# Optimization experiments

Measured on AMD Instinct MI355X. Metric: run time of the kernel, lower is better.

## Reference

```python
import jax, jax.numpy as jnp
import numpy as np

N, E = 50000, 1250000
IN_DIM, H, C, EDGE_DIM = 128, 2, 32, 64
NEG_SLOPE = 0.2


def setup_inputs() -> dict:
    key = jax.random.key(0)
    ks = jax.random.split(key, 9)
    x = jax.random.normal(ks[0], (N, IN_DIM), dtype=jnp.float32)
    edge_index = jax.random.randint(ks[1], (2, E), 0, N, dtype=jnp.int64)
    edge_attr = jax.random.normal(ks[2], (E, EDGE_DIM), dtype=jnp.float32)
    # learned params (PyG GATConv: glorot-style scale)
    W = jax.random.normal(ks[3], (IN_DIM, H * C), dtype=jnp.float32) * (1.0 / np.sqrt(IN_DIM))
    W_edge = jax.random.normal(ks[4], (EDGE_DIM, H * C), dtype=jnp.float32) * (1.0 / np.sqrt(EDGE_DIM))
    att_src = jax.random.normal(ks[5], (H, C), dtype=jnp.float32) * (1.0 / np.sqrt(C))
    att_dst = jax.random.normal(ks[6], (H, C), dtype=jnp.float32) * (1.0 / np.sqrt(C))
    att_edge = jax.random.normal(ks[7], (H, C), dtype=jnp.float32) * (1.0 / np.sqrt(C))
    bias = jnp.zeros((H * C,), dtype=jnp.float32)
    return {"x": x, "edge_index": edge_index, "edge_attr": edge_attr,
            "W": W, "W_edge": W_edge, "att_src": att_src, "att_dst": att_dst,
            "att_edge": att_edge, "bias": bias}


def reference(x, edge_index, edge_attr, W, W_edge, att_src, att_dst, att_edge, bias):
    # IntraGraphAttention.forward: relu then GATConv(in, 32, heads=2, edge_dim=64)
    x = jax.nn.relu(x)
    src, dst = edge_index[0], edge_index[1]

    # PyG add_self_loops(fill_value='mean'): self-loop edge_attr = mean of
    # incoming edge attrs per node (zeros for isolated nodes).
    deg = jax.ops.segment_sum(jnp.ones((E,), jnp.float32), dst, num_segments=N)
    loop_attr = jax.ops.segment_sum(edge_attr, dst, num_segments=N) / jnp.maximum(deg, 1.0)[:, None]
    loop_idx = jnp.arange(N, dtype=src.dtype)
    src_f = jnp.concatenate([src, loop_idx])          # [E+N]
    dst_f = jnp.concatenate([dst, loop_idx])          # [E+N]
    eattr_f = jnp.concatenate([edge_attr, loop_attr])  # [E+N, 64]

    # node / edge projections
    h = (x @ W).reshape(N, H, C)                       # [N,H,C]
    a_src = jnp.einsum('nhc,hc->nh', h, att_src)       # [N,H]
    a_dst = jnp.einsum('nhc,hc->nh', h, att_dst)       # [N,H]
    e = (eattr_f @ W_edge).reshape(-1, H, C)           # [E+N,H,C]
    a_edge = jnp.einsum('ehc,hc->eh', e, att_edge)     # [E+N,H]

    # per-edge attention logits
    alpha = a_src[src_f] + a_dst[dst_f] + a_edge       # [E+N,H]
    alpha = jax.nn.leaky_relu(alpha, NEG_SLOPE)

    # segment softmax over destination neighborhoods
    amax = jax.ops.segment_max(alpha, dst_f, num_segments=N)  # [N,H]
    p = jnp.exp(alpha - amax[dst_f])
    denom = jax.ops.segment_sum(p, dst_f, num_segments=N)     # [N,H]
    alpha = p / (denom[dst_f] + 1e-16)

    # scatter-aggregate messages (dropout dp=0 -> identity)
    msg = h[src_f] * alpha[..., None]                   # [E+N,H,C]
    out = jax.ops.segment_sum(msg, dst_f, num_segments=N)     # [N,H,C]
    return out.reshape(N, H * C) + bias
```

## Files before the change

### kernel.cpp

```cpp
#include <hip/hip_runtime.h>

#define NEG 0.2f

__global__ __launch_bounds__(256) void k_zero(int* __restrict__ p, int n) {
    int i = blockIdx.x * 256 + threadIdx.x;
    if (i < n) p[i] = 0;
}

__global__ __launch_bounds__(128) void k_node(
    const float* __restrict__ x, const float* __restrict__ W,
    const float* __restrict__ att_src, const float* __restrict__ att_dst,
    float* __restrict__ hbuf, float* __restrict__ a_src, float* __restrict__ a_dst, int N) {
    __shared__ float xs[128 * 36];
    __shared__ float Wl[128 * 64];
    const int t  = threadIdx.x;
    const int tn = t & 7;
    const int tc = t >> 3;
    const int node0 = blockIdx.x * 32;

    for (int j = t; j < 128 * 64; j += 128) Wl[j] = W[j];
    for (int j = t; j < 32 * 128; j += 128) {
        int n = j >> 7, k = j & 127;
        int nn = node0 + n;
        xs[k * 36 + n] = (nn < N) ? fmaxf(x[(size_t)nn * 128 + k], 0.f) : 0.f;
    }
    __syncthreads();

    float4 acc[4] = {{0,0,0,0},{0,0,0,0},{0,0,0,0},{0,0,0,0}};
#pragma unroll 8
    for (int k = 0; k < 128; ++k) {
        const float4 xv = *(const float4*)(xs + k * 36 + 4 * tn);
        const float4 wv = *(const float4*)(Wl + k * 64 + 4 * tc);
        acc[0].x = fmaf(xv.x, wv.x, acc[0].x); acc[0].y = fmaf(xv.x, wv.y, acc[0].y);
        acc[0].z = fmaf(xv.x, wv.z, acc[0].z); acc[0].w = fmaf(xv.x, wv.w, acc[0].w);
        acc[1].x = fmaf(xv.y, wv.x, acc[1].x); acc[1].y = fmaf(xv.y, wv.y, acc[1].y);
        acc[1].z = fmaf(xv.y, wv.z, acc[1].z); acc[1].w = fmaf(xv.y, wv.w, acc[1].w);
        acc[2].x = fmaf(xv.z, wv.x, acc[2].x); acc[2].y = fmaf(xv.z, wv.y, acc[2].y);
        acc[2].z = fmaf(xv.z, wv.z, acc[2].z); acc[2].w = fmaf(xv.z, wv.w, acc[2].w);
        acc[3].x = fmaf(xv.w, wv.x, acc[3].x); acc[3].y = fmaf(xv.w, wv.y, acc[3].y);
        acc[3].z = fmaf(xv.w, wv.z, acc[3].z); acc[3].w = fmaf(xv.w, wv.w, acc[3].w);
    }

#pragma unroll
    for (int n = 0; n < 4; ++n) {
        int nn = node0 + 4 * tn + n;
        if (nn < N) *(float4*)(hbuf + (size_t)nn * 64 + 4 * tc) = acc[n];
    }

    const float4 as4 = *(const float4*)(att_src + 4 * tc);
    const float4 ad4 = *(const float4*)(att_dst + 4 * tc);
    int head = (t >= 64) ? 1 : 0;
#pragma unroll
    for (int n = 0; n < 4; ++n) {
        float vs = acc[n].x * as4.x + acc[n].y * as4.y + acc[n].z * as4.z + acc[n].w * as4.w;
        float vd = acc[n].x * ad4.x + acc[n].y * ad4.y + acc[n].z * ad4.z + acc[n].w * ad4.w;
#pragma unroll
        for (int m = 8; m <= 32; m <<= 1) {
            vs += __shfl_xor(vs, m, 64);
            vd += __shfl_xor(vd, m, 64);
        }
        int nn = node0 + 4 * tn + n;
        if ((t & 63) < 8 && nn < N) {
            a_src[nn * 2 + head] = vs;
            a_dst[nn * 2 + head] = vd;
        }
    }
}

__global__ __launch_bounds__(256) void k_hist(
    const int* __restrict__ dstI, int* __restrict__ count, long long E,
    const float* __restrict__ W_edge, const float* __restrict__ att_edge,
    float* __restrict__ wke) {
    if (blockIdx.x == 0 && threadIdx.x < 128) {
        int hh = threadIdx.x >> 6;
        int k  = threadIdx.x & 63;
        float s = 0.f;
#pragma unroll
        for (int c = 0; c < 32; ++c)
            s += W_edge[k * 64 + hh * 32 + c] * att_edge[hh * 32 + c];
        wke[hh * 64 + k] = s;
    }
    long long i0 = (long long)blockIdx.x * 256 + threadIdx.x;
    long long stride = (long long)gridDim.x * 256;
    for (long long i = i0; i < E; i += stride)
        atomicAdd(&count[dstI[i]], 1);
}

__global__ __launch_bounds__(256) void k_scan1(const int* __restrict__ cnt, int* __restrict__ offs,
                                               int* __restrict__ bsum, int N) {
    __shared__ int ts[256];
    int t = threadIdx.x, blk = blockIdx.x;
    int base = blk * 1024 + t * 4;
    int v[4], s = 0;
#pragma unroll
    for (int i = 0; i < 4; ++i) {
        int idx = base + i;
        v[i] = (idx < N) ? cnt[idx] : 0;
        s += v[i];
    }
    ts[t] = s;
    __syncthreads();
    for (int off = 1; off < 256; off <<= 1) {
        int y = (t >= off) ? ts[t - off] : 0;
        __syncthreads();
        ts[t] += y;
        __syncthreads();
    }
    int run = ts[t] - s;
#pragma unroll
    for (int i = 0; i < 4; ++i) {
        int idx = base + i;
        if (idx < N) offs[idx] = run;
        run += v[i];
    }
    if (t == 255) bsum[blk] = ts[255];
}

__global__ void k_scan2(int* __restrict__ bsum, int nb) {
    int t = threadIdx.x;
    int orig = (t < nb) ? bsum[t] : 0;
    int v = orig;
#pragma unroll
    for (int off = 1; off < 64; off <<= 1) {
        int y = __shfl_up(v, off, 64);
        if (t >= off) v += y;
    }
    if (t < nb) bsum[t] = v - orig;
}

__global__ void k_scan3(int* __restrict__ offs, const int* __restrict__ bsum,
                        int* __restrict__ cursor, int N) {
    int idx = blockIdx.x * 256 + threadIdx.x;
    if (idx < N) {
        int o = offs[idx] + bsum[idx >> 10];
        offs[idx] = o;
        cursor[idx] = o;
    }
}

__global__ __launch_bounds__(256) void k_pa(
    const float* __restrict__ edge_attr, const int* __restrict__ srcI,
    const int* __restrict__ dstI, const float* __restrict__ wke,
    int* __restrict__ cursor, float4* __restrict__ evec, long long E) {
    __shared__ float wkes[128];
    if (threadIdx.x < 128) wkes[threadIdx.x] = wke[threadIdx.x];
    __syncthreads();
    long long i0 = (long long)blockIdx.x * 256 + threadIdx.x;
    long long stride = (long long)gridDim.x * 256;
    for (long long e = i0; e < E; e += stride) {
        const float4* row = (const float4*)(edge_attr + e * 64);
        float pa0 = 0.f, pa1 = 0.f;
#pragma unroll
        for (int k = 0; k < 16; ++k) {
            float4 ea = row[k];
            float4 wa = *(const float4*)(wkes + k * 4);
            float4 wb = *(const float4*)(wkes + 64 + k * 4);
            pa0 += ea.x * wa.x + ea.y * wa.y + ea.z * wa.z + ea.w * wa.w;
            pa1 += ea.x * wb.x + ea.y * wb.y + ea.z * wb.z + ea.w * wb.w;
        }
        int s = srcI[e], d = dstI[e];
        int pos = atomicAdd(&cursor[d], 1);
        evec[pos] = make_float4(pa0, pa1, __int_as_float(s), 0.f);
    }
}

__global__ __launch_bounds__(256) void k_agg(
    const float4* __restrict__ evec, const int* __restrict__ offs,
    const int* __restrict__ count, const float* __restrict__ a_src,
    const float* __restrict__ a_dst, const float* __restrict__ hbuf,
    const float* __restrict__ bias, float* __restrict__ out, int N) {
    int t = threadIdx.x;
    int lane = t & 63;
    int sub = lane & 15;
    int grp = lane >> 4;
    int n = blockIdx.x * 4 + (t >> 6);
    if (n >= N) return;
    int cnt  = count[n];
    int base = offs[n];
    float ad0 = a_dst[n * 2 + 0], ad1 = a_dst[n * 2 + 1];
    float accx = 0.f, accy = 0.f, accz = 0.f, accw = 0.f;
    float den0 = 0.f, den1 = 0.f, sae0 = 0.f, sae1 = 0.f;

    if (cnt > 0) {
        int last = cnt - 1;
        float4 evA = evec[base + (grp < cnt ? grp : last)];
        float4 evB = evec[base + (grp + 4 < cnt ? grp + 4 : last)];
        int sA = __float_as_int(evA.z);
        int sB = __float_as_int(evB.z);
        float2 asA = *(const float2*)(a_src + 2 * (size_t)sA);
        float4 hvA = *(const float4*)(hbuf + (size_t)sA * 64 + sub * 4);
        for (int j = grp; j < cnt; j += 4) {
            int jc = j + 8 < cnt ? j + 8 : last;
            float4 evC = evec[base + jc];
            float2 asB = *(const float2*)(a_src + 2 * (size_t)sB);
            float4 hvB = *(const float4*)(hbuf + (size_t)sB * 64 + sub * 4);
            float l0 = asA.x + ad0 + evA.x; l0 = l0 > 0.f ? l0 : NEG * l0;
            float l1 = asA.y + ad1 + evA.y; l1 = l1 > 0.f ? l1 : NEG * l1;
            float q0 = __expf(l0), q1 = __expf(l1);
            float q = (sub < 8) ? q0 : q1;
            accx = fmaf(q, hvA.x, accx);
            accy = fmaf(q, hvA.y, accy);
            accz = fmaf(q, hvA.z, accz);
            accw = fmaf(q, hvA.w, accw);
            den0 += q0; den1 += q1;
            sae0 += evA.x; sae1 += evA.y;
            evA = evB; sA = sB; asA = asB; hvA = hvB;
            evB = evC; sB = __float_as_int(evC.z);
        }
    }
#define RED2(v) { v += __shfl_xor(v, 16, 64); v += __shfl_xor(v, 32, 64); }
    RED2(accx) RED2(accy) RED2(accz) RED2(accw)
    RED2(den0) RED2(den1) RED2(sae0) RED2(sae1)
#undef RED2

    float dg = (cnt > 0) ? (float)cnt : 1.f;
    float as0 = a_src[n * 2 + 0], as1 = a_src[n * 2 + 1];
    float l0 = as0 + ad0 + sae0 / dg; l0 = l0 > 0.f ? l0 : NEG * l0;
    float l1 = as1 + ad1 + sae1 / dg; l1 = l1 > 0.f ? l1 : NEG * l1;
    float pl0 = __expf(l0), pl1 = __expf(l1);
    const float4 hn = *(const float4*)(hbuf + (size_t)n * 64 + sub * 4);
    float pl  = (sub < 8) ? pl0 : pl1;
    float den = ((sub < 8) ? den0 + pl0 : den1 + pl1) + 1e-16f;
    const float4 bv = *(const float4*)(bias + sub * 4);
    if (grp == 0) {
        float4 o;
        o.x = (accx + pl * hn.x) / den + bv.x;
        o.y = (accy + pl * hn.y) / den + bv.y;
        o.z = (accz + pl * hn.z) / den + bv.z;
        o.w = (accw + pl * hn.w) / den + bv.w;
        *(float4*)(out + (size_t)n * 64 + sub * 4) = o;
    }
}

extern "C" void kernel_launch(void* const* d_in, const int* in_sizes, int n_in,
                              void* d_out, int out_size, void* d_ws, size_t ws_size,
                              hipStream_t stream) {
    const float* x         = (const float*)d_in[0];
    const int*   ei        = (const int*)d_in[1];
    const float* edge_attr = (const float*)d_in[2];
    const float* W         = (const float*)d_in[3];
    const float* W_edge    = (const float*)d_in[4];
    const float* att_src   = (const float*)d_in[5];
    const float* att_dst   = (const float*)d_in[6];
    const float* att_edge  = (const float*)d_in[7];
    const float* bias      = (const float*)d_in[8];

    int N = in_sizes[0] / 128;
    long long E = in_sizes[1] / 2;
    const int* srcI = ei;
    const int* dstI = ei + E;

    char* ws = (char*)d_ws;
    float4* evec  = (float4*)ws;                      ws += (size_t)E * 16;
    float* wke    = (float*)ws;                       ws += 128 * 4;
    float* hbuf   = (float*)ws;                       ws += (size_t)N * 64 * 4;
    float* a_src  = (float*)ws;                       ws += (size_t)N * 2 * 4;
    float* a_dst  = (float*)ws;                       ws += (size_t)N * 2 * 4;
    int*   count  = (int*)ws;                         ws += (size_t)N * 4;
    int*   offs   = (int*)ws;                         ws += (size_t)N * 4;
    int*   cursor = (int*)ws;                         ws += (size_t)N * 4;
    int*   bsum   = (int*)ws;                         ws += 64 * 4;

    k_zero<<<(N + 255) / 256, 256, 0, stream>>>(count, N);
    k_node<<<(N + 31) / 32, 128, 0, stream>>>(x, W, att_src, att_dst, hbuf, a_src, a_dst, N);
    k_hist<<<2048, 256, 0, stream>>>(dstI, count, E, W_edge, att_edge, wke);

    int nb = (N + 1023) / 1024;
    k_scan1<<<nb, 256, 0, stream>>>(count, offs, bsum, N);
    k_scan2<<<1, 64, 0, stream>>>(bsum, nb);
    k_scan3<<<(N + 255) / 256, 256, 0, stream>>>(offs, bsum, cursor, N);

    k_pa<<<2048, 256, 0, stream>>>(edge_attr, srcI, dstI, wke, cursor, evec, E);

    k_agg<<<(N + 3) / 4, 256, 0, stream>>>(evec, offs, count, a_src, a_dst, hbuf, bias,
                                           (float*)d_out, N);
}
```

Measured before the change: 295.5 us.

## Fuse edge-attribute projection into aggregation and sort only edge indices

The separate pass that projected each edge's 64-dim attributes and scattered float4 records into destination order is replaced by a lighter sort that scatters only (edge id, src) int2 pairs. The aggregation kernel now gathers each edge's attribute row by edge id, computes the two head projections per 16-lane group, and reduces them with xor shuffles. This cuts the intermediate edge buffer write and read in half and drops one full streaming pass. In exchange, the 256-byte attribute rows are read in random order, which adds latency to an already gather-heavy aggregation loop that prefetches only one edge ahead, and each edge now costs extra shuffles.

```diff
diff --git a/kernel.cpp b/kernel.cpp
--- a/kernel.cpp
+++ b/kernel.cpp
@@ -138,38 +138,28 @@
     }
 }
 
-__global__ __launch_bounds__(256) void k_pa(
-    const float* __restrict__ edge_attr, const int* __restrict__ srcI,
-    const int* __restrict__ dstI, const float* __restrict__ wke,
-    int* __restrict__ cursor, float4* __restrict__ evec, long long E) {
-    __shared__ float wkes[128];
-    if (threadIdx.x < 128) wkes[threadIdx.x] = wke[threadIdx.x];
-    __syncthreads();
+__global__ __launch_bounds__(256) void k_sort(
+    const int* __restrict__ srcI, const int* __restrict__ dstI,
+    int* __restrict__ cursor, int2* __restrict__ epos, long long E) {
     long long i0 = (long long)blockIdx.x * 256 + threadIdx.x;
     long long stride = (long long)gridDim.x * 256;
     for (long long e = i0; e < E; e += stride) {
-        const float4* row = (const float4*)(edge_attr + e * 64);
-        float pa0 = 0.f, pa1 = 0.f;
-#pragma unroll
-        for (int k = 0; k < 16; ++k) {
-            float4 ea = row[k];
-            float4 wa = *(const float4*)(wkes + k * 4);
-            float4 wb = *(const float4*)(wkes + 64 + k * 4);
-            pa0 += ea.x * wa.x + ea.y * wa.y + ea.z * wa.z + ea.w * wa.w;
-            pa1 += ea.x * wb.x + ea.y * wb.y + ea.z * wb.z + ea.w * wb.w;
-        }
         int s = srcI[e], d = dstI[e];
         int pos = atomicAdd(&cursor[d], 1);
-        evec[pos] = make_float4(pa0, pa1, __int_as_float(s), 0.f);
+        epos[pos] = make_int2((int)e, s);
     }
 }
 
 __global__ __launch_bounds__(256) void k_agg(
-    const float4* __restrict__ evec, const int* __restrict__ offs,
-    const int* __restrict__ count, const float* __restrict__ a_src,
+    const int2* __restrict__ epos, const int* __restrict__ offs,
+    const int* __restrict__ count, const float* __restrict__ edge_attr,
+    const float* __restrict__ wke, const float* __restrict__ a_src,
     const float* __restrict__ a_dst, const float* __restrict__ hbuf,
     const float* __restrict__ bias, float* __restrict__ out, int N) {
+    __shared__ float wkes[128];
     int t = threadIdx.x;
+    if (t < 128) wkes[t] = wke[t];
+    __syncthreads();
     int lane = t & 63;
     int sub = lane & 15;
     int grp = lane >> 4;
@@ -177,25 +167,34 @@
     if (n >= N) return;
     int cnt  = count[n];
     int base = offs[n];
+    const float4 wa = *(const float4*)(wkes + sub * 4);
+    const float4 wb = *(const float4*)(wkes + 64 + sub * 4);
     float ad0 = a_dst[n * 2 + 0], ad1 = a_dst[n * 2 + 1];
     float accx = 0.f, accy = 0.f, accz = 0.f, accw = 0.f;
     float den0 = 0.f, den1 = 0.f, sae0 = 0.f, sae1 = 0.f;
 
     if (cnt > 0) {
         int last = cnt - 1;
-        float4 evA = evec[base + (grp < cnt ? grp : last)];
-        float4 evB = evec[base + (grp + 4 < cnt ? grp + 4 : last)];
-        int sA = __float_as_int(evA.z);
-        int sB = __float_as_int(evB.z);
-        float2 asA = *(const float2*)(a_src + 2 * (size_t)sA);
-        float4 hvA = *(const float4*)(hbuf + (size_t)sA * 64 + sub * 4);
+        int2 epA = epos[base + (grp < cnt ? grp : last)];
+        int2 epB = epos[base + (grp + 4 < cnt ? grp + 4 : last)];
+        float4 eaA = *(const float4*)(edge_attr + (size_t)epA.x * 64 + sub * 4);
+        float2 asA = *(const float2*)(a_src + 2 * (size_t)epA.y);
+        float4 hvA = *(const float4*)(hbuf + (size_t)epA.y * 64 + sub * 4);
         for (int j = grp; j < cnt; j += 4) {
             int jc = j + 8 < cnt ? j + 8 : last;
-            float4 evC = evec[base + jc];
-            float2 asB = *(const float2*)(a_src + 2 * (size_t)sB);
-            float4 hvB = *(const float4*)(hbuf + (size_t)sB * 64 + sub * 4);
-            float l0 = asA.x + ad0 + evA.x; l0 = l0 > 0.f ? l0 : NEG * l0;
-            float l1 = asA.y + ad1 + evA.y; l1 = l1 > 0.f ? l1 : NEG * l1;
+            int2 epC = epos[base + jc];
+            float4 eaB = *(const float4*)(edge_attr + (size_t)epB.x * 64 + sub * 4);
+            float2 asB = *(const float2*)(a_src + 2 * (size_t)epB.y);
+            float4 hvB = *(const float4*)(hbuf + (size_t)epB.y * 64 + sub * 4);
+            float pa0 = eaA.x * wa.x + eaA.y * wa.y + eaA.z * wa.z + eaA.w * wa.w;
+            float pa1 = eaA.x * wb.x + eaA.y * wb.y + eaA.z * wb.z + eaA.w * wb.w;
+#pragma unroll
+            for (int m = 1; m <= 8; m <<= 1) {
+                pa0 += __shfl_xor(pa0, m, 64);
+                pa1 += __shfl_xor(pa1, m, 64);
+            }
+            float l0 = asA.x + ad0 + pa0; l0 = l0 > 0.f ? l0 : NEG * l0;
+            float l1 = asA.y + ad1 + pa1; l1 = l1 > 0.f ? l1 : NEG * l1;
             float q0 = __expf(l0), q1 = __expf(l1);
             float q = (sub < 8) ? q0 : q1;
             accx = fmaf(q, hvA.x, accx);
@@ -203,9 +202,9 @@
             accz = fmaf(q, hvA.z, accz);
             accw = fmaf(q, hvA.w, accw);
             den0 += q0; den1 += q1;
-            sae0 += evA.x; sae1 += evA.y;
-            evA = evB; sA = sB; asA = asB; hvA = hvB;
-            evB = evC; sB = __float_as_int(evC.z);
+            sae0 += pa0; sae1 += pa1;
+            epA = epB; eaA = eaB; asA = asB; hvA = hvB;
+            epB = epC;
         }
     }
 #define RED2(v) { v += __shfl_xor(v, 16, 64); v += __shfl_xor(v, 32, 64); }
@@ -251,7 +250,7 @@
     const int* dstI = ei + E;
 
     char* ws = (char*)d_ws;
-    float4* evec  = (float4*)ws;                      ws += (size_t)E * 16;
+    int2*  epos   = (int2*)ws;                        ws += (size_t)E * 8;
     float* wke    = (float*)ws;                       ws += 128 * 4;
     float* hbuf   = (float*)ws;                       ws += (size_t)N * 64 * 4;
     float* a_src  = (float*)ws;                       ws += (size_t)N * 2 * 4;
@@ -270,8 +269,8 @@
     k_scan2<<<1, 64, 0, stream>>>(bsum, nb);
     k_scan3<<<(N + 255) / 256, 256, 0, stream>>>(offs, bsum, cursor, N);
 
-    k_pa<<<2048, 256, 0, stream>>>(edge_attr, srcI, dstI, wke, cursor, evec, E);
-
-    k_agg<<<(N + 3) / 4, 256, 0, stream>>>(evec, offs, count, a_src, a_dst, hbuf, bias,
-                                           (float*)d_out, N);
-}
+    k_sort<<<2048, 256, 0, stream>>>(srcI, dstI, cursor, epos, E);
+
+    k_agg<<<(N + 3) / 4, 256, 0, stream>>>(epos, offs, count, edge_attr, wke, a_src, a_dst,
+                                           hbuf, bias, (float*)d_out, N);
+}
```

After: 334.4 us. +13.1%, slower.

## Bucket edges by groups of 8 destinations and aggregate via LDS atomics

Applied to the files above, without the earlier changes.

Replaces the per-node CSR sort with coarse buckets of eight destination nodes. Counting, scanning and partitioning now work on buckets, with a single-block scan in place of the three-kernel scan, and the zeroing and wke setup are folded into the node kernel. Each wave handles one bucket and accumulates messages, denominators and self-loop sums through shared-memory float atomics. This cuts kernel launches and global atomic contention on cursors. In exchange it adds LDS atomic traffic, non-deterministic summation order, and a wider payload that also carries the destination.

```diff
diff --git a/kernel.cpp b/kernel.cpp
--- a/kernel.cpp
+++ b/kernel.cpp
@@ -1,19 +1,29 @@
 #include <hip/hip_runtime.h>
 
 #define NEG 0.2f
-
-__global__ __launch_bounds__(256) void k_zero(int* __restrict__ p, int n) {
-    int i = blockIdx.x * 256 + threadIdx.x;
-    if (i < n) p[i] = 0;
-}
+#define NPB 8
 
 __global__ __launch_bounds__(128) void k_node(
     const float* __restrict__ x, const float* __restrict__ W,
     const float* __restrict__ att_src, const float* __restrict__ att_dst,
-    float* __restrict__ hbuf, float* __restrict__ a_src, float* __restrict__ a_dst, int N) {
+    const float* __restrict__ W_edge, const float* __restrict__ att_edge,
+    float* __restrict__ hbuf, float* __restrict__ a_src, float* __restrict__ a_dst,
+    float* __restrict__ wke, int* __restrict__ bcount, int N, int nbk) {
     __shared__ float xs[128 * 36];
     __shared__ float Wl[128 * 64];
     const int t  = threadIdx.x;
+
+    int gi = blockIdx.x * 128 + t;
+    if (gi < nbk) bcount[gi] = 0;
+    if (blockIdx.x == 0) {
+        int hh = t >> 6, k = t & 63;
+        float s = 0.f;
+#pragma unroll
+        for (int c = 0; c < 32; ++c)
+            s += W_edge[k * 64 + hh * 32 + c] * att_edge[hh * 32 + c];
+        wke[hh * 64 + k] = s;
+    }
+
     const int tn = t & 7;
     const int tc = t >> 3;
     const int node0 = blockIdx.x * 32;
@@ -67,36 +77,25 @@
     }
 }
 
-__global__ __launch_bounds__(256) void k_hist(
-    const int* __restrict__ dstI, int* __restrict__ count, long long E,
-    const float* __restrict__ W_edge, const float* __restrict__ att_edge,
-    float* __restrict__ wke) {
-    if (blockIdx.x == 0 && threadIdx.x < 128) {
-        int hh = threadIdx.x >> 6;
-        int k  = threadIdx.x & 63;
-        float s = 0.f;
-#pragma unroll
-        for (int c = 0; c < 32; ++c)
-            s += W_edge[k * 64 + hh * 32 + c] * att_edge[hh * 32 + c];
-        wke[hh * 64 + k] = s;
-    }
+__global__ __launch_bounds__(256) void k_cnt(const int* __restrict__ dstI,
+                                             int* __restrict__ bcount, long long E) {
     long long i0 = (long long)blockIdx.x * 256 + threadIdx.x;
     long long stride = (long long)gridDim.x * 256;
     for (long long i = i0; i < E; i += stride)
-        atomicAdd(&count[dstI[i]], 1);
-}
-
-__global__ __launch_bounds__(256) void k_scan1(const int* __restrict__ cnt, int* __restrict__ offs,
-                                               int* __restrict__ bsum, int N) {
+        atomicAdd(&bcount[dstI[i] >> 3], 1);
+}
+
+__global__ __launch_bounds__(256) void k_bscan(const int* __restrict__ bcount,
+                                               int* __restrict__ boffs,
+                                               int* __restrict__ bcursor, int nbk) {
     __shared__ int ts[256];
-    int t = threadIdx.x, blk = blockIdx.x;
-    int base = blk * 1024 + t * 4;
-    int v[4], s = 0;
-#pragma unroll
-    for (int i = 0; i < 4; ++i) {
+    int t = threadIdx.x;
+    int K = (nbk + 255) >> 8;
+    int base = t * K;
+    int s = 0;
+    for (int i = 0; i < K; ++i) {
         int idx = base + i;
-        v[i] = (idx < N) ? cnt[idx] : 0;
-        s += v[i];
+        s += (idx < nbk) ? bcount[idx] : 0;
     }
     ts[t] = s;
     __syncthreads();
@@ -107,41 +106,21 @@
         __syncthreads();
     }
     int run = ts[t] - s;
-#pragma unroll
-    for (int i = 0; i < 4; ++i) {
+    for (int i = 0; i < K; ++i) {
         int idx = base + i;
-        if (idx < N) offs[idx] = run;
-        run += v[i];
-    }
-    if (t == 255) bsum[blk] = ts[255];
-}
-
-__global__ void k_scan2(int* __restrict__ bsum, int nb) {
-    int t = threadIdx.x;
-    int orig = (t < nb) ? bsum[t] : 0;
-    int v = orig;
-#pragma unroll
-    for (int off = 1; off < 64; off <<= 1) {
-        int y = __shfl_up(v, off, 64);
-        if (t >= off) v += y;
-    }
-    if (t < nb) bsum[t] = v - orig;
-}
-
-__global__ void k_scan3(int* __restrict__ offs, const int* __restrict__ bsum,
-                        int* __restrict__ cursor, int N) {
-    int idx = blockIdx.x * 256 + threadIdx.x;
-    if (idx < N) {
-        int o = offs[idx] + bsum[idx >> 10];
-        offs[idx] = o;
-        cursor[idx] = o;
-    }
-}
-
-__global__ __launch_bounds__(256) void k_pa(
+        if (idx < nbk) {
+            int v = bcount[idx];
+            boffs[idx] = run;
+            bcursor[idx] = run;
+            run += v;
+        }
+    }
+}
+
+__global__ __launch_bounds__(256) void k_part(
     const float* __restrict__ edge_attr, const int* __restrict__ srcI,
     const int* __restrict__ dstI, const float* __restrict__ wke,
-    int* __restrict__ cursor, float4* __restrict__ evec, long long E) {
+    int* __restrict__ bcursor, int4* __restrict__ payload, long long E) {
     __shared__ float wkes[128];
     if (threadIdx.x < 128) wkes[threadIdx.x] = wke[threadIdx.x];
     __syncthreads();
@@ -159,76 +138,76 @@
             pa1 += ea.x * wb.x + ea.y * wb.y + ea.z * wb.z + ea.w * wb.w;
         }
         int s = srcI[e], d = dstI[e];
-        int pos = atomicAdd(&cursor[d], 1);
-        evec[pos] = make_float4(pa0, pa1, __int_as_float(s), 0.f);
-    }
-}
-
-__global__ __launch_bounds__(256) void k_agg(
-    const float4* __restrict__ evec, const int* __restrict__ offs,
-    const int* __restrict__ count, const float* __restrict__ a_src,
+        int pos = atomicAdd(&bcursor[d >> 3], 1);
+        payload[pos] = make_int4(__float_as_int(pa0), __float_as_int(pa1), s, d);
+    }
+}
+
+__global__ __launch_bounds__(256) void k_bucket(
+    const int4* __restrict__ payload, const int* __restrict__ boffs,
+    const int* __restrict__ bcount, const float* __restrict__ a_src,
     const float* __restrict__ a_dst, const float* __restrict__ hbuf,
-    const float* __restrict__ bias, float* __restrict__ out, int N) {
+    const float* __restrict__ bias, float* __restrict__ out, int N, int nbk) {
+    __shared__ float lds[4 * NPB * 70];
     int t = threadIdx.x;
-    int lane = t & 63;
-    int sub = lane & 15;
-    int grp = lane >> 4;
-    int n = blockIdx.x * 4 + (t >> 6);
-    if (n >= N) return;
-    int cnt  = count[n];
-    int base = offs[n];
-    float ad0 = a_dst[n * 2 + 0], ad1 = a_dst[n * 2 + 1];
-    float accx = 0.f, accy = 0.f, accz = 0.f, accw = 0.f;
-    float den0 = 0.f, den1 = 0.f, sae0 = 0.f, sae1 = 0.f;
-
-    if (cnt > 0) {
-        int last = cnt - 1;
-        float4 evA = evec[base + (grp < cnt ? grp : last)];
-        float4 evB = evec[base + (grp + 4 < cnt ? grp + 4 : last)];
-        int sA = __float_as_int(evA.z);
-        int sB = __float_as_int(evB.z);
-        float2 asA = *(const float2*)(a_src + 2 * (size_t)sA);
-        float4 hvA = *(const float4*)(hbuf + (size_t)sA * 64 + sub * 4);
-        for (int j = grp; j < cnt; j += 4) {
-            int jc = j + 8 < cnt ? j + 8 : last;
-            float4 evC = evec[base + jc];
-            float2 asB = *(const float2*)(a_src + 2 * (size_t)sB);
-            float4 hvB = *(const float4*)(hbuf + (size_t)sB * 64 + sub * 4);
-            float l0 = asA.x + ad0 + evA.x; l0 = l0 > 0.f ? l0 : NEG * l0;
-            float l1 = asA.y + ad1 + evA.y; l1 = l1 > 0.f ? l1 : NEG * l1;
-            float q0 = __expf(l0), q1 = __expf(l1);
-            float q = (sub < 8) ? q0 : q1;
-            accx = fmaf(q, hvA.x, accx);
-            accy = fmaf(q, hvA.y, accy);
-            accz = fmaf(q, hvA.z, accz);
-            accw = fmaf(q, hvA.w, accw);
-            den0 += q0; den1 += q1;
-            sae0 += evA.x; sae1 += evA.y;
-            evA = evB; sA = sB; asA = asB; hvA = hvB;
-            evB = evC; sB = __float_as_int(evC.z);
-        }
-    }
-#define RED2(v) { v += __shfl_xor(v, 16, 64); v += __shfl_xor(v, 32, 64); }
-    RED2(accx) RED2(accy) RED2(accz) RED2(accw)
-    RED2(den0) RED2(den1) RED2(sae0) RED2(sae1)
-#undef RED2
-
-    float dg = (cnt > 0) ? (float)cnt : 1.f;
-    float as0 = a_src[n * 2 + 0], as1 = a_src[n * 2 + 1];
-    float l0 = as0 + ad0 + sae0 / dg; l0 = l0 > 0.f ? l0 : NEG * l0;
-    float l1 = as1 + ad1 + sae1 / dg; l1 = l1 > 0.f ? l1 : NEG * l1;
-    float pl0 = __expf(l0), pl1 = __expf(l1);
-    const float4 hn = *(const float4*)(hbuf + (size_t)n * 64 + sub * 4);
-    float pl  = (sub < 8) ? pl0 : pl1;
-    float den = ((sub < 8) ? den0 + pl0 : den1 + pl1) + 1e-16f;
-    const float4 bv = *(const float4*)(bias + sub * 4);
-    if (grp == 0) {
-        float4 o;
-        o.x = (accx + pl * hn.x) / den + bv.x;
-        o.y = (accy + pl * hn.y) / den + bv.y;
-        o.z = (accz + pl * hn.z) / den + bv.z;
-        o.w = (accw + pl * hn.w) / den + bv.w;
-        *(float4*)(out + (size_t)n * 64 + sub * 4) = o;
+    int w = t >> 6, lane = t & 63;
+    int g = lane >> 4, c = lane & 15;
+    int bk = blockIdx.x * 4 + w;
+    if (bk >= nbk) return;
+    float* L = lds + w * NPB * 70;
+    for (int i = lane; i < NPB * 70; i += 64) L[i] = 0.f;
+
+    int beg = boffs[bk], cnt = bcount[bk];
+    float bv = bias[lane];
+
+    for (int j = 0; j < cnt; j += 4) {
+        int je = j + g;
+        bool v = je < cnt;
+        int4 pl = payload[beg + (v ? je : 0)];
+        float pa0 = __int_as_float(pl.x), pa1 = __int_as_float(pl.y);
+        int s = pl.z, d = pl.w;
+        int dl = d & (NPB - 1);
+        float2 as2 = *(const float2*)(a_src + 2 * (size_t)s);
+        float2 ad2 = *(const float2*)(a_dst + 2 * (size_t)d);
+        float4 hv = *(const float4*)(hbuf + (size_t)s * 64 + c * 4);
+        float l0 = as2.x + ad2.x + pa0; l0 = l0 > 0.f ? l0 : NEG * l0;
+        float l1 = as2.y + ad2.y + pa1; l1 = l1 > 0.f ? l1 : NEG * l1;
+        float q0 = __expf(l0), q1 = __expf(l1);
+        float q = (c < 8) ? q0 : q1;
+        if (v) {
+            float* ap = L + dl * 70 + c * 4;
+            atomicAdd(ap + 0, q * hv.x);
+            atomicAdd(ap + 1, q * hv.y);
+            atomicAdd(ap + 2, q * hv.z);
+            atomicAdd(ap + 3, q * hv.w);
+            if (c == 0) {
+                float* sp = L + dl * 70 + 64;
+                atomicAdd(sp + 0, q0);
+                atomicAdd(sp + 1, q1);
+                atomicAdd(sp + 2, pa0);
+                atomicAdd(sp + 3, pa1);
+                atomicAdd(sp + 4, 1.f);
+            }
+        }
+    }
+
+    for (int nl = 0; nl < NPB; ++nl) {
+        int n = bk * NPB + nl;
+        if (n >= N) break;
+        float accv = L[nl * 70 + lane];
+        float den0 = L[nl * 70 + 64], den1 = L[nl * 70 + 65];
+        float sae0 = L[nl * 70 + 66], sae1 = L[nl * 70 + 67];
+        float dg   = L[nl * 70 + 68];
+        float dgm  = dg > 0.f ? dg : 1.f;
+        float as0 = a_src[n * 2 + 0], as1 = a_src[n * 2 + 1];
+        float ad0 = a_dst[n * 2 + 0], ad1 = a_dst[n * 2 + 1];
+        float l0 = as0 + ad0 + sae0 / dgm; l0 = l0 > 0.f ? l0 : NEG * l0;
+        float l1 = as1 + ad1 + sae1 / dgm; l1 = l1 > 0.f ? l1 : NEG * l1;
+        float pl0 = __expf(l0), pl1 = __expf(l1);
+        float hn = hbuf[(size_t)n * 64 + lane];
+        float plx = (lane < 32) ? pl0 : pl1;
+        float den = ((lane < 32) ? den0 + pl0 : den1 + pl1) + 1e-16f;
+        out[(size_t)n * 64 + lane] = (accv + plx * hn) / den + bv;
     }
 }
 
@@ -249,29 +228,24 @@
     long long E = in_sizes[1] / 2;
     const int* srcI = ei;
     const int* dstI = ei + E;
+    int nbk = (N + NPB - 1) / NPB;
 
     char* ws = (char*)d_ws;
-    float4* evec  = (float4*)ws;                      ws += (size_t)E * 16;
-    float* wke    = (float*)ws;                       ws += 128 * 4;
-    float* hbuf   = (float*)ws;                       ws += (size_t)N * 64 * 4;
-    float* a_src  = (float*)ws;                       ws += (size_t)N * 2 * 4;
-    float* a_dst  = (float*)ws;                       ws += (size_t)N * 2 * 4;
-    int*   count  = (int*)ws;                         ws += (size_t)N * 4;
-    int*   offs   = (int*)ws;                         ws += (size_t)N * 4;
-    int*   cursor = (int*)ws;                         ws += (size_t)N * 4;
-    int*   bsum   = (int*)ws;                         ws += 64 * 4;
-
-    k_zero<<<(N + 255) / 256, 256, 0, stream>>>(count, N);
-    k_node<<<(N + 31) / 32, 128, 0, stream>>>(x, W, att_src, att_dst, hbuf, a_src, a_dst, N);
-    k_hist<<<2048, 256, 0, stream>>>(dstI, count, E, W_edge, att_edge, wke);
-
-    int nb = (N + 1023) / 1024;
-    k_scan1<<<nb, 256, 0, stream>>>(count, offs, bsum, N);
-    k_scan2<<<1, 64, 0, stream>>>(bsum, nb);
-    k_scan3<<<(N + 255) / 256, 256, 0, stream>>>(offs, bsum, cursor, N);
-
-    k_pa<<<2048, 256, 0, stream>>>(edge_attr, srcI, dstI, wke, cursor, evec, E);
-
-    k_agg<<<(N + 3) / 4, 256, 0, stream>>>(evec, offs, count, a_src, a_dst, hbuf, bias,
-                                           (float*)d_out, N);
-}
+    int4*  payload = (int4*)ws;                ws += (size_t)E * 16;
+    float* hbuf    = (float*)ws;               ws += (size_t)N * 64 * 4;
+    float* a_src   = (float*)ws;               ws += (size_t)N * 2 * 4;
+    float* a_dst   = (float*)ws;               ws += (size_t)N * 2 * 4;
+    float* wke     = (float*)ws;               ws += 128 * 4;
+    int*   bcount  = (int*)ws;                 ws += (size_t)nbk * 4;
+    int*   boffs   = (int*)ws;                 ws += (size_t)nbk * 4;
+    int*   bcursor = (int*)ws;                 ws += (size_t)nbk * 4;
+
+    int nblk_node = (N + 31) / 32;
+    k_node<<<nblk_node, 128, 0, stream>>>(x, W, att_src, att_dst, W_edge, att_edge,
+                                          hbuf, a_src, a_dst, wke, bcount, N, nbk);
+    k_cnt<<<2048, 256, 0, stream>>>(dstI, bcount, E);
+    k_bscan<<<1, 256, 0, stream>>>(bcount, boffs, bcursor, nbk);
+    k_part<<<2048, 256, 0, stream>>>(edge_attr, srcI, dstI, wke, bcursor, payload, E);
+    k_bucket<<<(nbk + 3) / 4, 256, 0, stream>>>(payload, boffs, bcount, a_src, a_dst,
+                                                hbuf, bias, (float*)d_out, N, nbk);
+}
```

Result: slower. 745.5 us (+152.3%).
